# Performance work log

Hardware: AMD Instinct MI355X
Metric: run time of the kernel (lower is better)

## Reference

```python
import jax, jax.numpy as jnp
import numpy as np

K_TOP = 8
TEMP = 1.0
GUMBEL_EPS = 1e-20
GEN_EPS = 1e-7
NEG_INF = -1e9


def _genconv(xn, src, dst, e, We, be, W1, b1, W2, b2):
    """GENConv: edge-proj, m=relu(x_src+e)+eps, per-dst softmax aggregation (t=1),
    residual add, then 2-layer MLP."""
    N = xn.shape[0]
    ep = e @ We + be                         # [E, C]
    m = jax.nn.relu(xn[src] + ep) + GEN_EPS  # [E, C]
    mx = jax.ops.segment_max(m, dst, num_segments=N)
    mx = jnp.where(jnp.isfinite(mx), mx, 0.0)
    w = jnp.exp(m - mx[dst])
    den = jax.ops.segment_sum(w, dst, num_segments=N)
    agg = jax.ops.segment_sum(w * m, dst, num_segments=N) / jnp.where(den > 0, den, 1.0)
    out = agg + xn
    return jax.nn.relu(out @ W1 + b1) @ W2 + b2


def setup_inputs() -> dict:
    key = jax.random.key(0)
    ks = jax.random.split(key, 16)
    N, E, D, ED = 1024, 16384, 128, 16
    H1, H2, OUT = 64, 64, 40
    s = 0.02
    return {
        "x": jax.random.normal(ks[0], (N, D), jnp.float32),
        "edge_attr": jax.random.normal(ks[1], (E, ED), jnp.float32),
        "gumbel_u": jax.random.uniform(ks[2], (N, N), jnp.float32),
        "mlp_w": jax.random.normal(ks[3], (ED + 2 * D, 1), jnp.float32) * s,
        "mlp_b": jnp.zeros((1,), jnp.float32),
        "c1_we": jax.random.normal(ks[4], (ED, D), jnp.float32) * s,
        "c1_be": jnp.zeros((D,), jnp.float32),
        "c1_w1": jax.random.normal(ks[5], (D, 2 * D), jnp.float32) * s,
        "c1_b1": jnp.zeros((2 * D,), jnp.float32),
        "c1_w2": jax.random.normal(ks[6], (2 * D, H1), jnp.float32) * s,
        "c1_b2": jnp.zeros((H1,), jnp.float32),
        "c2_we": jax.random.normal(ks[7], (ED, H1), jnp.float32) * s,
        "c2_be": jnp.zeros((H1,), jnp.float32),
        "c2_w1": jax.random.normal(ks[8], (H1, 2 * H1), jnp.float32) * s,
        "c2_b1": jnp.zeros((2 * H1,), jnp.float32),
        "c2_w2": jax.random.normal(ks[9], (2 * H1, H2), jnp.float32) * s,
        "c2_b2": jnp.zeros((H2,), jnp.float32),
        "fc_w": jax.random.normal(ks[10], (H2, OUT), jnp.float32) * s,
        "fc_b": jnp.zeros((OUT,), jnp.float32),
        "num_nodes": N,
        "edge_index": jax.random.randint(ks[11], (2, E), 0, N),
        "node_mask": jnp.ones((N,), jnp.int32),
    }


def reference(x, edge_attr, gumbel_u, mlp_w, mlp_b,
              c1_we, c1_be, c1_w1, c1_b1, c1_w2, c1_b2,
              c2_we, c2_be, c2_w1, c2_b1, c2_w2, c2_b2,
              fc_w, fc_b, num_nodes, edge_index, node_mask):
    N, D = x.shape
    src, dst = edge_index[0], edge_index[1]

    # dense adjacency (duplicate edges sum, only used as a zero/nonzero mask)
    adj = jnp.zeros((N, N), x.dtype).at[src, dst].add(1.0)

    # Edge-score MLP on concat([x_u, x_v*mask, edge_attr_dense]) decomposed
    # linearly (same math as scoring the dense [N,N,2D+ED] feature tensor).
    w_node, w_nb, w_e = mlp_w[:D], mlp_w[D:2 * D], mlp_w[2 * D:]
    s_edge = jnp.zeros((N, N), x.dtype).at[src, dst].set((edge_attr @ w_e)[:, 0])
    score = (x @ w_node) + (x @ w_nb).T * (adj > 0) + s_edge + mlp_b[0]
    score = jnp.where(adj == 0, NEG_INF, score)

    z = jax.nn.softmax(score, axis=-1)
    g = -jnp.log(-jnp.log(gumbel_u + GUMBEL_EPS) + GUMBEL_EPS)
    z = jax.nn.softmax((z + g) / TEMP, axis=-1)

    # top-k edge sampling; softmax output is strictly positive so valid_mask
    # (z>0) is always all-True and shapes stay static at N*k edges.
    _, topi = jax.lax.top_k(z, K_TOP)                       # [N, k]
    new_src = jnp.repeat(jnp.arange(N), K_TOP)
    new_dst = topi.reshape(-1)

    # match each new edge against old edge list (argmax of boolean equality,
    # unmatched edges fall back to index 0 exactly as torch argmax does)
    eq = (edge_index[0][None, :] == new_src[:, None]) & \
         (edge_index[1][None, :] == new_dst[:, None])       # [N*k, E]
    new_attr = edge_attr[jnp.argmax(eq, axis=-1)]

    h = _genconv(x, new_src, new_dst, new_attr, c1_we, c1_be, c1_w1, c1_b1, c1_w2, c1_b2)
    h = jax.nn.relu(h)
    h = _genconv(h, new_src, new_dst, new_attr, c2_we, c2_be, c2_w1, c2_b1, c2_w2, c2_b2)
    h = jax.nn.relu(h)
    out = h @ fc_w + fc_b
    # node_mask is all ones, so x[node_mask != 0] == identity; masked write
    # keeps static shapes under jit.
    return jnp.where((node_mask != 0)[:, None], out, 0.0)
```

## Files before the change

kernel.cpp:

```cpp
#include <hip/hip_runtime.h>
#include <cfloat>

#define NN   1024
#define NE   16384
#define D0   128
#define EDIM 16
#define NH1  64
#define NOUT 40
#define KTOP 8
#define NEGINF (-1000000000.0f)

#define OFF_A    0u
#define OFF_B    4096u
#define OFF_DST  8192u
#define OFF_EM   40960u
#define OFF_H    73728u

__device__ __forceinline__ void amx(float& v, int& j, float ov, int oj) {
    if (ov > v || (ov == v && oj < j)) { v = ov; j = oj; }
}

__global__ __launch_bounds__(256) void ab_kernel(
    const float* __restrict__ x, const float* __restrict__ mlp_w,
    float* __restrict__ a, float* __restrict__ b)
{
    int t = threadIdx.x, lane = t & 63, wid = t >> 6;
    int row = blockIdx.x * 4 + wid;
    const float* xr = x + row * D0;
    float x0 = xr[lane], x1 = xr[64 + lane];
    float sa = x0 * mlp_w[lane]       + x1 * mlp_w[64 + lane];
    float sb = x0 * mlp_w[128 + lane] + x1 * mlp_w[192 + lane];
    for (int s = 32; s; s >>= 1) { sa += __shfl_down(sa, s); sb += __shfl_down(sb, s); }
    if (lane == 0) { a[row] = sa; b[row] = sb; }
}

__global__ __launch_bounds__(256) void row_topk_kernel(
    const float* __restrict__ ea, const float* __restrict__ mlp_w,
    const float* __restrict__ mlp_b, const float* __restrict__ a,
    const float* __restrict__ b, const float* __restrict__ u,
    const int* __restrict__ ei, int* __restrict__ dsti, int* __restrict__ em)
{
    __shared__ float sv[NN];
    __shared__ int   idmx[NN];
    __shared__ int   idmn[NN];
    __shared__ float wred[4];
    __shared__ int   wredj[4];
    const int i = blockIdx.x, t = threadIdx.x;
    const int lane = t & 63, wid = t >> 6;

    for (int j = t; j < NN; j += 256) { idmx[j] = -1; idmn[j] = 0x7FFFFFFF; }
    __syncthreads();
    for (int e = t; e < NE; e += 256) {
        if (ei[e] == i) {
            int dj = ei[NE + e];
            atomicMax(&idmx[dj], e);
            atomicMin(&idmn[dj], e);
        }
    }
    __syncthreads();

    float we[EDIM];
    #pragma unroll
    for (int k = 0; k < EDIM; k++) we[k] = mlp_w[2 * D0 + k];
    const float bias = mlp_b[0];
    const float ai = a[i];

    float lmax = NEGINF;
    for (int j = t; j < NN; j += 256) {
        int id = idmx[j];
        float s;
        if (id >= 0) {
            float se = 0.f;
            #pragma unroll
            for (int k = 0; k < EDIM; k++) se += ea[id * EDIM + k] * we[k];
            s = ((ai + b[j]) + se) + bias;
        } else {
            s = NEGINF;
        }
        sv[j] = s;
        lmax = fmaxf(lmax, s);
    }
    for (int s = 32; s; s >>= 1) lmax = fmaxf(lmax, __shfl_down(lmax, s));
    if (lane == 0) wred[wid] = lmax;
    __syncthreads();
    float rowmax = fmaxf(fmaxf(wred[0], wred[1]), fmaxf(wred[2], wred[3]));
    bool noedge = (rowmax == NEGINF);
    __syncthreads();

    float lsum = 0.f;
    for (int j = t; j < NN; j += 256) {
        float evv;
        if (noedge) evv = 1.0f;
        else { float s = sv[j]; evv = (s == NEGINF) ? 0.0f : expf(s - rowmax); }
        sv[j] = evv;
        lsum += evv;
    }
    for (int s = 32; s; s >>= 1) lsum += __shfl_down(lsum, s);
    if (lane == 0) wred[wid] = lsum;
    __syncthreads();
    float rsum = wred[0] + wred[1] + wred[2] + wred[3];
    __syncthreads();

    for (int j = t; j < NN; j += 256) {
        float z = sv[j] / rsum;
        float uu = u[i * NN + j];
        float g = -logf(-logf(uu + 1e-20f) + 1e-20f);
        sv[j] = z + g;
    }
    __syncthreads();

    for (int sel = 0; sel < KTOP; sel++) {
        float bv = -FLT_MAX; int bj = NN;
        for (int j = t; j < NN; j += 256) amx(bv, bj, sv[j], j);
        for (int s = 32; s; s >>= 1) {
            float ov = __shfl_down(bv, s); int oj = __shfl_down(bj, s);
            amx(bv, bj, ov, oj);
        }
        if (lane == 0) { wred[wid] = bv; wredj[wid] = bj; }
        __syncthreads();
        if (t == 0) {
            float v = wred[0]; int j = wredj[0];
            amx(v, j, wred[1], wredj[1]);
            amx(v, j, wred[2], wredj[2]);
            amx(v, j, wred[3], wredj[3]);
            dsti[i * KTOP + sel] = j;
            int mn = idmn[j];
            em[i * KTOP + sel] = (mn == 0x7FFFFFFF) ? 0 : mn;
            sv[j] = -FLT_MAX;
        }
        __syncthreads();
    }
}

__global__ __launch_bounds__(128) void genconv1_kernel(
    const float* __restrict__ x, const float* __restrict__ ea,
    const float* __restrict__ we_g, const float* __restrict__ be,
    const float* __restrict__ w1, const float* __restrict__ b1,
    const float* __restrict__ w2, const float* __restrict__ b2,
    const int* __restrict__ dsti, const int* __restrict__ em,
    float* __restrict__ h)
{
    __shared__ int   slots[256];
    __shared__ float eatt[256 * EDIM];
    __shared__ float arow[D0];
    __shared__ float t1[2 * D0];
    __shared__ int   lcnt;
    const int r = blockIdx.x, t = threadIdx.x;
    if (t == 0) lcnt = 0;
    __syncthreads();
    for (int n = t; n < NN * KTOP; n += 128)
        if (dsti[n] == r) { int p = atomicAdd(&lcnt, 1); if (p < 256) slots[p] = n; }
    __syncthreads();
    int cnt = min(lcnt, 256);
    if (t == 0) {
        for (int p = 1; p < cnt; p++) {
            int v = slots[p]; int q = p - 1;
            while (q >= 0 && slots[q] > v) { slots[q + 1] = slots[q]; q--; }
            slots[q + 1] = v;
        }
    }
    __syncthreads();
    for (int q = t; q < cnt * EDIM; q += 128)
        eatt[q] = ea[em[slots[q >> 4]] * EDIM + (q & 15)];
    __syncthreads();

    const int d = t;
    float wed[EDIM];
    #pragma unroll
    for (int k = 0; k < EDIM; k++) wed[k] = we_g[k * D0 + d];
    const float bed = be[d];

    float mxv = -FLT_MAX;
    for (int idx = 0; idx < cnt; idx++) {
        int n = slots[idx]; int src = n >> 3;
        float ep = bed;
        #pragma unroll
        for (int k = 0; k < EDIM; k++) ep += eatt[idx * EDIM + k] * wed[k];
        float m = fmaxf(x[src * D0 + d] + ep, 0.f) + 1e-7f;
        mxv = fmaxf(mxv, m);
    }
    float den = 0.f, num = 0.f;
    for (int idx = 0; idx < cnt; idx++) {
        int n = slots[idx]; int src = n >> 3;
        float ep = bed;
        #pragma unroll
        for (int k = 0; k < EDIM; k++) ep += eatt[idx * EDIM + k] * wed[k];
        float m = fmaxf(x[src * D0 + d] + ep, 0.f) + 1e-7f;
        float w = expf(m - mxv);
        den += w; num += w * m;
    }
    float agg = cnt ? num / (den > 0.f ? den : 1.f) : 0.f;
    arow[d] = agg + x[r * D0 + d];
    __syncthreads();

    float acc0 = b1[d], acc1 = b1[d + D0];
    for (int k = 0; k < D0; k++) {
        float av = arow[k];
        acc0 += av * w1[k * 2 * D0 + d];
        acc1 += av * w1[k * 2 * D0 + d + D0];
    }
    t1[d] = fmaxf(acc0, 0.f);
    t1[d + D0] = fmaxf(acc1, 0.f);
    __syncthreads();
    if (t < NH1) {
        float acc = b2[t];
        for (int k = 0; k < 2 * D0; k++) acc += t1[k] * w2[k * NH1 + t];
        h[r * NH1 + t] = fmaxf(acc, 0.f);
    }
}

__global__ __launch_bounds__(128) void genconv2_kernel(
    const float* __restrict__ h, const float* __restrict__ ea,
    const float* __restrict__ we_g, const float* __restrict__ be,
    const float* __restrict__ w1, const float* __restrict__ b1,
    const float* __restrict__ w2, const float* __restrict__ b2,
    const float* __restrict__ fcw, const float* __restrict__ fcb,
    const int* __restrict__ dsti, const int* __restrict__ em,
    const int* __restrict__ mask, float* __restrict__ out)
{
    __shared__ int   slots[256];
    __shared__ float eatt[256 * EDIM];
    __shared__ float arow[NH1];
    __shared__ float t2[2 * NH1];
    __shared__ float h2[NH1];
    __shared__ int   lcnt;
    const int r = blockIdx.x, t = threadIdx.x;
    if (t == 0) lcnt = 0;
    __syncthreads();
    for (int n = t; n < NN * KTOP; n += 128)
        if (dsti[n] == r) { int p = atomicAdd(&lcnt, 1); if (p < 256) slots[p] = n; }
    __syncthreads();
    int cnt = min(lcnt, 256);
    if (t == 0) {
        for (int p = 1; p < cnt; p++) {
            int v = slots[p]; int q = p - 1;
            while (q >= 0 && slots[q] > v) { slots[q + 1] = slots[q]; q--; }
            slots[q + 1] = v;
        }
    }
    __syncthreads();
    for (int q = t; q < cnt * EDIM; q += 128)
        eatt[q] = ea[em[slots[q >> 4]] * EDIM + (q & 15)];
    __syncthreads();

    if (t < NH1) {
        const int d = t;
        float wed[EDIM];
        #pragma unroll
        for (int k = 0; k < EDIM; k++) wed[k] = we_g[k * NH1 + d];
        const float bed = be[d];
        float mxv = -FLT_MAX;
        for (int idx = 0; idx < cnt; idx++) {
            int n = slots[idx]; int src = n >> 3;
            float ep = bed;
            #pragma unroll
            for (int k = 0; k < EDIM; k++) ep += eatt[idx * EDIM + k] * wed[k];
            float m = fmaxf(h[src * NH1 + d] + ep, 0.f) + 1e-7f;
            mxv = fmaxf(mxv, m);
        }
        float den = 0.f, num = 0.f;
        for (int idx = 0; idx < cnt; idx++) {
            int n = slots[idx]; int src = n >> 3;
            float ep = bed;
            #pragma unroll
            for (int k = 0; k < EDIM; k++) ep += eatt[idx * EDIM + k] * wed[k];
            float m = fmaxf(h[src * NH1 + d] + ep, 0.f) + 1e-7f;
            float w = expf(m - mxv);
            den += w; num += w * m;
        }
        float agg = cnt ? num / (den > 0.f ? den : 1.f) : 0.f;
        arow[d] = agg + h[r * NH1 + d];
    }
    __syncthreads();

    {
        float acc = b1[t];
        for (int k = 0; k < NH1; k++) acc += arow[k] * w1[k * 2 * NH1 + t];
        t2[t] = fmaxf(acc, 0.f);
    }
    __syncthreads();
    if (t < NH1) {
        float acc = b2[t];
        for (int k = 0; k < 2 * NH1; k++) acc += t2[k] * w2[k * NH1 + t];
        h2[t] = fmaxf(acc, 0.f);
    }
    __syncthreads();
    if (t < NOUT) {
        float acc = fcb[t];
        for (int k = 0; k < NH1; k++) acc += h2[k] * fcw[k * NOUT + t];
        out[r * NOUT + t] = (mask[r] != 0) ? acc : 0.f;
    }
}

extern "C" void kernel_launch(void* const* d_in, const int* in_sizes, int n_in,
                              void* d_out, int out_size, void* d_ws, size_t ws_size,
                              hipStream_t stream) {
    const float* x      = (const float*)d_in[0];
    const float* ea     = (const float*)d_in[1];
    const float* u      = (const float*)d_in[2];
    const float* mlp_w  = (const float*)d_in[3];
    const float* mlp_b  = (const float*)d_in[4];
    const float* c1_we  = (const float*)d_in[5];
    const float* c1_be  = (const float*)d_in[6];
    const float* c1_w1  = (const float*)d_in[7];
    const float* c1_b1  = (const float*)d_in[8];
    const float* c1_w2  = (const float*)d_in[9];
    const float* c1_b2  = (const float*)d_in[10];
    const float* c2_we  = (const float*)d_in[11];
    const float* c2_be  = (const float*)d_in[12];
    const float* c2_w1  = (const float*)d_in[13];
    const float* c2_b1  = (const float*)d_in[14];
    const float* c2_w2  = (const float*)d_in[15];
    const float* c2_b2  = (const float*)d_in[16];
    const float* fc_w   = (const float*)d_in[17];
    const float* fc_b   = (const float*)d_in[18];
    const int*   ei     = (const int*)d_in[20];
    const int*   mask   = (const int*)d_in[21];

    char* ws = (char*)d_ws;
    float* a    = (float*)(ws + OFF_A);
    float* b    = (float*)(ws + OFF_B);
    int*   dsti = (int*)(ws + OFF_DST);
    int*   em   = (int*)(ws + OFF_EM);
    float* h    = (float*)(ws + OFF_H);
    float* out  = (float*)d_out;

    ab_kernel<<<NN / 4, 256, 0, stream>>>(x, mlp_w, a, b);
    row_topk_kernel<<<NN, 256, 0, stream>>>(ea, mlp_w, mlp_b, a, b, u, ei, dsti, em);
    genconv1_kernel<<<NN, 128, 0, stream>>>(x, ea, c1_we, c1_be, c1_w1, c1_b1, c1_w2, c1_b2,
                                            dsti, em, h);
    genconv2_kernel<<<NN, 128, 0, stream>>>(h, ea, c2_we, c2_be, c2_w1, c2_b1, c2_w2, c2_b2,
                                            fc_w, fc_b, dsti, em, mask, out);
}
```

Before: 192.0 us.

## Build dense edge-id matrices and CSR incoming lists instead of per-block edge scans

Replaces each row_topk block's scan of all 16384 edges with a global dense N×N edge-id max/min table built once by atomics, and precomputes per-edge attribute scores. Adds a single-block CSR builder, so the genconv kernels read their incoming-edge lists instead of each scanning all N*k destinations. The genconv kernels now pack 2 or 4 nodes per block. This adds an 8 MB memset and a large, sparsely read table, and caps in-degree at 64, which could truncate high-degree nodes.

```diff
diff --git a/kernel.cpp b/kernel.cpp
--- a/kernel.cpp
+++ b/kernel.cpp
@@ -9,74 +9,73 @@
 #define NOUT 40
 #define KTOP 8
 #define NEGINF (-1000000000.0f)
-
-#define OFF_A    0u
-#define OFF_B    4096u
-#define OFF_DST  8192u
-#define OFF_EM   40960u
-#define OFF_H    73728u
+#define MAXDEG 64
+
+#define OFF_IDMAX 0u
+#define OFF_IDMIN 4194304u
+#define OFF_SE    8388608u
+#define OFF_A     8454144u
+#define OFF_B     8458240u
+#define OFF_DST   8462336u
+#define OFF_EM    8495104u
+#define OFF_RS    8527872u
+#define OFF_SLOT  8536064u
+#define OFF_H     8568832u
 
 __device__ __forceinline__ void amx(float& v, int& j, float ov, int oj) {
     if (ov > v || (ov == v && oj < j)) { v = ov; j = oj; }
 }
 
-__global__ __launch_bounds__(256) void ab_kernel(
-    const float* __restrict__ x, const float* __restrict__ mlp_w,
-    float* __restrict__ a, float* __restrict__ b)
-{
-    int t = threadIdx.x, lane = t & 63, wid = t >> 6;
-    int row = blockIdx.x * 4 + wid;
-    const float* xr = x + row * D0;
-    float x0 = xr[lane], x1 = xr[64 + lane];
-    float sa = x0 * mlp_w[lane]       + x1 * mlp_w[64 + lane];
-    float sb = x0 * mlp_w[128 + lane] + x1 * mlp_w[192 + lane];
-    for (int s = 32; s; s >>= 1) { sa += __shfl_down(sa, s); sb += __shfl_down(sb, s); }
-    if (lane == 0) { a[row] = sa; b[row] = sb; }
+__global__ __launch_bounds__(256) void prep_kernel(
+    const float* __restrict__ x, const float* __restrict__ ea,
+    const float* __restrict__ mlp_w, const int* __restrict__ ei,
+    int* __restrict__ idmax, unsigned* __restrict__ idmin,
+    float* __restrict__ se, float* __restrict__ a, float* __restrict__ b)
+{
+    int bid = blockIdx.x, t = threadIdx.x;
+    if (bid < 64) {
+        int e = bid * 256 + t;
+        int s = ei[e], d = ei[NE + e];
+        atomicMax(idmax + s * NN + d, e);
+        atomicMin(idmin + s * NN + d, (unsigned)e);
+        float acc = 0.f;
+        #pragma unroll
+        for (int k = 0; k < EDIM; k++) acc += ea[e * EDIM + k] * mlp_w[2 * D0 + k];
+        se[e] = acc;
+    } else {
+        int lane = t & 63, wid = t >> 6;
+        int row = (bid - 64) * 4 + wid;
+        const float* xr = x + row * D0;
+        float x0 = xr[lane], x1 = xr[64 + lane];
+        float sa = x0 * mlp_w[lane]       + x1 * mlp_w[64 + lane];
+        float sb = x0 * mlp_w[128 + lane] + x1 * mlp_w[192 + lane];
+        for (int s2 = 32; s2; s2 >>= 1) { sa += __shfl_down(sa, s2); sb += __shfl_down(sb, s2); }
+        if (lane == 0) { a[row] = sa; b[row] = sb; }
+    }
 }
 
 __global__ __launch_bounds__(256) void row_topk_kernel(
-    const float* __restrict__ ea, const float* __restrict__ mlp_w,
-    const float* __restrict__ mlp_b, const float* __restrict__ a,
-    const float* __restrict__ b, const float* __restrict__ u,
-    const int* __restrict__ ei, int* __restrict__ dsti, int* __restrict__ em)
+    const int* __restrict__ idmax, const unsigned* __restrict__ idmin,
+    const float* __restrict__ se, const float* __restrict__ mlp_b,
+    const float* __restrict__ a, const float* __restrict__ b,
+    const float* __restrict__ u, int* __restrict__ dsti, int* __restrict__ em)
 {
     __shared__ float sv[NN];
-    __shared__ int   idmx[NN];
-    __shared__ int   idmn[NN];
+    __shared__ unsigned idl[NN];
     __shared__ float wred[4];
     __shared__ int   wredj[4];
     const int i = blockIdx.x, t = threadIdx.x;
     const int lane = t & 63, wid = t >> 6;
-
-    for (int j = t; j < NN; j += 256) { idmx[j] = -1; idmn[j] = 0x7FFFFFFF; }
-    __syncthreads();
-    for (int e = t; e < NE; e += 256) {
-        if (ei[e] == i) {
-            int dj = ei[NE + e];
-            atomicMax(&idmx[dj], e);
-            atomicMin(&idmn[dj], e);
-        }
-    }
-    __syncthreads();
-
-    float we[EDIM];
-    #pragma unroll
-    for (int k = 0; k < EDIM; k++) we[k] = mlp_w[2 * D0 + k];
+    const int rowoff = i * NN;
     const float bias = mlp_b[0];
     const float ai = a[i];
 
     float lmax = NEGINF;
-    for (int j = t; j < NN; j += 256) {
-        int id = idmx[j];
-        float s;
-        if (id >= 0) {
-            float se = 0.f;
-            #pragma unroll
-            for (int k = 0; k < EDIM; k++) se += ea[id * EDIM + k] * we[k];
-            s = ((ai + b[j]) + se) + bias;
-        } else {
-            s = NEGINF;
-        }
+    #pragma unroll
+    for (int q = 0; q < 4; q++) {
+        int j = t + q * 256;
+        int id = idmax[rowoff + j];
+        float s = (id >= 0) ? (((ai + b[j]) + se[id]) + bias) : NEGINF;
         sv[j] = s;
         lmax = fmaxf(lmax, s);
     }
@@ -88,12 +87,15 @@
     __syncthreads();
 
     float lsum = 0.f;
-    for (int j = t; j < NN; j += 256) {
+    #pragma unroll
+    for (int q = 0; q < 4; q++) {
+        int j = t + q * 256;
         float evv;
         if (noedge) evv = 1.0f;
         else { float s = sv[j]; evv = (s == NEGINF) ? 0.0f : expf(s - rowmax); }
         sv[j] = evv;
         lsum += evv;
+        idl[j] = idmin[rowoff + j];
     }
     for (int s = 32; s; s >>= 1) lsum += __shfl_down(lsum, s);
     if (lane == 0) wred[wid] = lsum;
@@ -101,9 +103,11 @@
     float rsum = wred[0] + wred[1] + wred[2] + wred[3];
     __syncthreads();
 
-    for (int j = t; j < NN; j += 256) {
+    #pragma unroll
+    for (int q = 0; q < 4; q++) {
+        int j = t + q * 256;
         float z = sv[j] / rsum;
-        float uu = u[i * NN + j];
+        float uu = u[rowoff + j];
         float g = -logf(-logf(uu + 1e-20f) + 1e-20f);
         sv[j] = z + g;
     }
@@ -111,7 +115,8 @@
 
     for (int sel = 0; sel < KTOP; sel++) {
         float bv = -FLT_MAX; int bj = NN;
-        for (int j = t; j < NN; j += 256) amx(bv, bj, sv[j], j);
+        #pragma unroll
+        for (int q = 0; q < 4; q++) { int j = t + q * 256; amx(bv, bj, sv[j], j); }
         for (int s = 32; s; s >>= 1) {
             float ov = __shfl_down(bv, s); int oj = __shfl_down(bj, s);
             amx(bv, bj, ov, oj);
@@ -124,47 +129,82 @@
             amx(v, j, wred[2], wredj[2]);
             amx(v, j, wred[3], wredj[3]);
             dsti[i * KTOP + sel] = j;
-            int mn = idmn[j];
-            em[i * KTOP + sel] = (mn == 0x7FFFFFFF) ? 0 : mn;
+            unsigned mn = idl[j];
+            em[i * KTOP + sel] = (mn == 0xFFFFFFFFu) ? 0 : (int)mn;
             sv[j] = -FLT_MAX;
         }
         __syncthreads();
     }
 }
 
-__global__ __launch_bounds__(128) void genconv1_kernel(
+__global__ __launch_bounds__(1024) void csr_kernel(
+    const int* __restrict__ dsti, int* __restrict__ rs, int* __restrict__ slot)
+{
+    __shared__ int cnts[NN];
+    __shared__ int sc[NN];
+    __shared__ int ptr[NN];
+    const int t = threadIdx.x;
+    cnts[t] = 0;
+    __syncthreads();
+    int dloc[8];
+    #pragma unroll
+    for (int q = 0; q < 8; q++) {
+        dloc[q] = dsti[q * NN + t];
+        atomicAdd(&cnts[dloc[q]], 1);
+    }
+    __syncthreads();
+    int v = cnts[t];
+    sc[t] = v;
+    __syncthreads();
+    for (int off = 1; off < NN; off <<= 1) {
+        int add = (t >= off) ? sc[t - off] : 0;
+        __syncthreads();
+        sc[t] += add;
+        __syncthreads();
+    }
+    int excl = sc[t] - v;
+    rs[t] = excl;
+    if (t == NN - 1) rs[NN] = NE / 2;
+    ptr[t] = excl;
+    __syncthreads();
+    #pragma unroll
+    for (int q = 0; q < 8; q++) {
+        int n = q * NN + t;
+        int p = atomicAdd(&ptr[dloc[q]], 1);
+        slot[p] = n;
+    }
+}
+
+__global__ __launch_bounds__(256) void genconv1_kernel(
     const float* __restrict__ x, const float* __restrict__ ea,
     const float* __restrict__ we_g, const float* __restrict__ be,
     const float* __restrict__ w1, const float* __restrict__ b1,
     const float* __restrict__ w2, const float* __restrict__ b2,
-    const int* __restrict__ dsti, const int* __restrict__ em,
-    float* __restrict__ h)
-{
-    __shared__ int   slots[256];
-    __shared__ float eatt[256 * EDIM];
-    __shared__ float arow[D0];
-    __shared__ float t1[2 * D0];
-    __shared__ int   lcnt;
-    const int r = blockIdx.x, t = threadIdx.x;
-    if (t == 0) lcnt = 0;
-    __syncthreads();
-    for (int n = t; n < NN * KTOP; n += 128)
-        if (dsti[n] == r) { int p = atomicAdd(&lcnt, 1); if (p < 256) slots[p] = n; }
-    __syncthreads();
-    int cnt = min(lcnt, 256);
-    if (t == 0) {
+    const int* __restrict__ rs, const int* __restrict__ slot,
+    const int* __restrict__ em, float* __restrict__ h)
+{
+    __shared__ int   slots[2][MAXDEG];
+    __shared__ float eatt[2][MAXDEG * EDIM];
+    __shared__ float arow[2][D0];
+    __shared__ float t1s[2][2 * D0];
+    const int t = threadIdx.x, sub = t >> 7, d = t & 127;
+    const int r = blockIdx.x * 2 + sub;
+    const int beg = rs[r];
+    const int cnt = min(rs[r + 1] - beg, MAXDEG);
+    if (d < cnt) slots[sub][d] = slot[beg + d];
+    __syncthreads();
+    if (d == 0) {
         for (int p = 1; p < cnt; p++) {
-            int v = slots[p]; int q = p - 1;
-            while (q >= 0 && slots[q] > v) { slots[q + 1] = slots[q]; q--; }
-            slots[q + 1] = v;
-        }
-    }
-    __syncthreads();
-    for (int q = t; q < cnt * EDIM; q += 128)
-        eatt[q] = ea[em[slots[q >> 4]] * EDIM + (q & 15)];
-    __syncthreads();
-
-    const int d = t;
+            int v = slots[sub][p]; int q = p - 1;
+            while (q >= 0 && slots[sub][q] > v) { slots[sub][q + 1] = slots[sub][q]; q--; }
+            slots[sub][q + 1] = v;
+        }
+    }
+    __syncthreads();
+    for (int q = d; q < cnt * EDIM; q += 128)
+        eatt[sub][q] = ea[em[slots[sub][q >> 4]] * EDIM + (q & 15)];
+    __syncthreads();
+
     float wed[EDIM];
     #pragma unroll
     for (int k = 0; k < EDIM; k++) wed[k] = we_g[k * D0 + d];
@@ -172,123 +212,125 @@
 
     float mxv = -FLT_MAX;
     for (int idx = 0; idx < cnt; idx++) {
-        int n = slots[idx]; int src = n >> 3;
+        int src = slots[sub][idx] >> 3;
         float ep = bed;
         #pragma unroll
-        for (int k = 0; k < EDIM; k++) ep += eatt[idx * EDIM + k] * wed[k];
+        for (int k = 0; k < EDIM; k++) ep += eatt[sub][idx * EDIM + k] * wed[k];
         float m = fmaxf(x[src * D0 + d] + ep, 0.f) + 1e-7f;
         mxv = fmaxf(mxv, m);
     }
     float den = 0.f, num = 0.f;
     for (int idx = 0; idx < cnt; idx++) {
-        int n = slots[idx]; int src = n >> 3;
+        int src = slots[sub][idx] >> 3;
         float ep = bed;
         #pragma unroll
-        for (int k = 0; k < EDIM; k++) ep += eatt[idx * EDIM + k] * wed[k];
+        for (int k = 0; k < EDIM; k++) ep += eatt[sub][idx * EDIM + k] * wed[k];
         float m = fmaxf(x[src * D0 + d] + ep, 0.f) + 1e-7f;
         float w = expf(m - mxv);
         den += w; num += w * m;
     }
     float agg = cnt ? num / (den > 0.f ? den : 1.f) : 0.f;
-    arow[d] = agg + x[r * D0 + d];
+    arow[sub][d] = agg + x[r * D0 + d];
     __syncthreads();
 
     float acc0 = b1[d], acc1 = b1[d + D0];
     for (int k = 0; k < D0; k++) {
-        float av = arow[k];
+        float av = arow[sub][k];
         acc0 += av * w1[k * 2 * D0 + d];
         acc1 += av * w1[k * 2 * D0 + d + D0];
     }
-    t1[d] = fmaxf(acc0, 0.f);
-    t1[d + D0] = fmaxf(acc1, 0.f);
-    __syncthreads();
-    if (t < NH1) {
-        float acc = b2[t];
-        for (int k = 0; k < 2 * D0; k++) acc += t1[k] * w2[k * NH1 + t];
-        h[r * NH1 + t] = fmaxf(acc, 0.f);
-    }
-}
-
-__global__ __launch_bounds__(128) void genconv2_kernel(
+    t1s[sub][d] = fmaxf(acc0, 0.f);
+    t1s[sub][d + D0] = fmaxf(acc1, 0.f);
+    __syncthreads();
+    if (d < NH1) {
+        float acc = b2[d];
+        for (int k = 0; k < 2 * D0; k++) acc += t1s[sub][k] * w2[k * NH1 + d];
+        h[r * NH1 + d] = fmaxf(acc, 0.f);
+    }
+}
+
+__global__ __launch_bounds__(256) void genconv2_kernel(
     const float* __restrict__ h, const float* __restrict__ ea,
     const float* __restrict__ we_g, const float* __restrict__ be,
     const float* __restrict__ w1, const float* __restrict__ b1,
     const float* __restrict__ w2, const float* __restrict__ b2,
     const float* __restrict__ fcw, const float* __restrict__ fcb,
-    const int* __restrict__ dsti, const int* __restrict__ em,
-    const int* __restrict__ mask, float* __restrict__ out)
-{
-    __shared__ int   slots[256];
-    __shared__ float eatt[256 * EDIM];
-    __shared__ float arow[NH1];
-    __shared__ float t2[2 * NH1];
-    __shared__ float h2[NH1];
-    __shared__ int   lcnt;
-    const int r = blockIdx.x, t = threadIdx.x;
-    if (t == 0) lcnt = 0;
-    __syncthreads();
-    for (int n = t; n < NN * KTOP; n += 128)
-        if (dsti[n] == r) { int p = atomicAdd(&lcnt, 1); if (p < 256) slots[p] = n; }
-    __syncthreads();
-    int cnt = min(lcnt, 256);
-    if (t == 0) {
+    const int* __restrict__ rs, const int* __restrict__ slot,
+    const int* __restrict__ em, const int* __restrict__ mask,
+    float* __restrict__ out)
+{
+    __shared__ int   slots[4][MAXDEG];
+    __shared__ float eatt[4][MAXDEG * EDIM];
+    __shared__ float arow[4][NH1];
+    __shared__ float t2s[4][2 * NH1];
+    __shared__ float h2s[4][NH1];
+    const int t = threadIdx.x, sub = t >> 6, d = t & 63;
+    const int r = blockIdx.x * 4 + sub;
+    const int beg = rs[r];
+    const int cnt = min(rs[r + 1] - beg, MAXDEG);
+    if (d < cnt) slots[sub][d] = slot[beg + d];
+    __syncthreads();
+    if (d == 0) {
         for (int p = 1; p < cnt; p++) {
-            int v = slots[p]; int q = p - 1;
-            while (q >= 0 && slots[q] > v) { slots[q + 1] = slots[q]; q--; }
-            slots[q + 1] = v;
-        }
-    }
-    __syncthreads();
-    for (int q = t; q < cnt * EDIM; q += 128)
-        eatt[q] = ea[em[slots[q >> 4]] * EDIM + (q & 15)];
-    __syncthreads();
-
-    if (t < NH1) {
-        const int d = t;
-        float wed[EDIM];
-        #pragma unroll
-        for (int k = 0; k < EDIM; k++) wed[k] = we_g[k * NH1 + d];
-        const float bed = be[d];
-        float mxv = -FLT_MAX;
-        for (int idx = 0; idx < cnt; idx++) {
-            int n = slots[idx]; int src = n >> 3;
-            float ep = bed;
-            #pragma unroll
-            for (int k = 0; k < EDIM; k++) ep += eatt[idx * EDIM + k] * wed[k];
-            float m = fmaxf(h[src * NH1 + d] + ep, 0.f) + 1e-7f;
-            mxv = fmaxf(mxv, m);
-        }
-        float den = 0.f, num = 0.f;
-        for (int idx = 0; idx < cnt; idx++) {
-            int n = slots[idx]; int src = n >> 3;
-            float ep = bed;
-            #pragma unroll
-            for (int k = 0; k < EDIM; k++) ep += eatt[idx * EDIM + k] * wed[k];
-            float m = fmaxf(h[src * NH1 + d] + ep, 0.f) + 1e-7f;
-            float w = expf(m - mxv);
-            den += w; num += w * m;
-        }
-        float agg = cnt ? num / (den > 0.f ? den : 1.f) : 0.f;
-        arow[d] = agg + h[r * NH1 + d];
-    }
+            int v = slots[sub][p]; int q = p - 1;
+            while (q >= 0 && slots[sub][q] > v) { slots[sub][q + 1] = slots[sub][q]; q--; }
+            slots[sub][q + 1] = v;
+        }
+    }
+    __syncthreads();
+    for (int q = d; q < cnt * EDIM; q += 64)
+        eatt[sub][q] = ea[em[slots[sub][q >> 4]] * EDIM + (q & 15)];
+    __syncthreads();
+
+    float wed[EDIM];
+    #pragma unroll
+    for (int k = 0; k < EDIM; k++) wed[k] = we_g[k * NH1 + d];
+    const float bed = be[d];
+
+    float mxv = -FLT_MAX;
+    for (int idx = 0; idx < cnt; idx++) {
+        int src = slots[sub][idx] >> 3;
+        float ep = bed;
+        #pragma unroll
+        for (int k = 0; k < EDIM; k++) ep += eatt[sub][idx * EDIM + k] * wed[k];
+        float m = fmaxf(h[src * NH1 + d] + ep, 0.f) + 1e-7f;
+        mxv = fmaxf(mxv, m);
+    }
+    float den = 0.f, num = 0.f;
+    for (int idx = 0; idx < cnt; idx++) {
+        int src = slots[sub][idx] >> 3;
+        float ep = bed;
+        #pragma unroll
+        for (int k = 0; k < EDIM; k++) ep += eatt[sub][idx * EDIM + k] * wed[k];
+        float m = fmaxf(h[src * NH1 + d] + ep, 0.f) + 1e-7f;
+        float w = expf(m - mxv);
+        den += w; num += w * m;
+    }
+    float agg = cnt ? num / (den > 0.f ? den : 1.f) : 0.f;
+    arow[sub][d] = agg + h[r * NH1 + d];
     __syncthreads();
 
     {
-        float acc = b1[t];
-        for (int k = 0; k < NH1; k++) acc += arow[k] * w1[k * 2 * NH1 + t];
-        t2[t] = fmaxf(acc, 0.f);
-    }
-    __syncthreads();
-    if (t < NH1) {
-        float acc = b2[t];
-        for (int k = 0; k < 2 * NH1; k++) acc += t2[k] * w2[k * NH1 + t];
-        h2[t] = fmaxf(acc, 0.f);
-    }
-    __syncthreads();
-    if (t < NOUT) {
-        float acc = fcb[t];
-        for (int k = 0; k < NH1; k++) acc += h2[k] * fcw[k * NOUT + t];
-        out[r * NOUT + t] = (mask[r] != 0) ? acc : 0.f;
+        float acc_a = b1[d], acc_b = b1[d + NH1];
+        for (int k = 0; k < NH1; k++) {
+            float av = arow[sub][k];
+            acc_a += av * w1[k * 2 * NH1 + d];
+            acc_b += av * w1[k * 2 * NH1 + d + NH1];
+        }
+        t2s[sub][d] = fmaxf(acc_a, 0.f);
+        t2s[sub][d + NH1] = fmaxf(acc_b, 0.f);
+    }
+    __syncthreads();
+    {
+        float acc = b2[d];
+        for (int k = 0; k < 2 * NH1; k++) acc += t2s[sub][k] * w2[k * NH1 + d];
+        h2s[sub][d] = fmaxf(acc, 0.f);
+    }
+    __syncthreads();
+    if (d < NOUT) {
+        float acc = fcb[d];
+        for (int k = 0; k < NH1; k++) acc += h2s[sub][k] * fcw[k * NOUT + d];
+        out[r * NOUT + d] = (mask[r] != 0) ? acc : 0.f;
     }
 }
 
@@ -318,17 +360,24 @@
     const int*   mask   = (const int*)d_in[21];
 
     char* ws = (char*)d_ws;
+    int*      idmax = (int*)(ws + OFF_IDMAX);
+    unsigned* idmin = (unsigned*)(ws + OFF_IDMIN);
+    float* se   = (float*)(ws + OFF_SE);
     float* a    = (float*)(ws + OFF_A);
     float* b    = (float*)(ws + OFF_B);
     int*   dsti = (int*)(ws + OFF_DST);
     int*   em   = (int*)(ws + OFF_EM);
+    int*   rs   = (int*)(ws + OFF_RS);
+    int*   slot = (int*)(ws + OFF_SLOT);
     float* h    = (float*)(ws + OFF_H);
     float* out  = (float*)d_out;
 
-    ab_kernel<<<NN / 4, 256, 0, stream>>>(x, mlp_w, a, b);
-    row_topk_kernel<<<NN, 256, 0, stream>>>(ea, mlp_w, mlp_b, a, b, u, ei, dsti, em);
-    genconv1_kernel<<<NN, 128, 0, stream>>>(x, ea, c1_we, c1_be, c1_w1, c1_b1, c1_w2, c1_b2,
-                                            dsti, em, h);
-    genconv2_kernel<<<NN, 128, 0, stream>>>(h, ea, c2_we, c2_be, c2_w1, c2_b1, c2_w2, c2_b2,
-                                            fc_w, fc_b, dsti, em, mask, out);
-}
+    hipMemsetAsync(ws + OFF_IDMAX, 0xFF, 8388608u, stream);
+    prep_kernel<<<320, 256, 0, stream>>>(x, ea, mlp_w, ei, idmax, idmin, se, a, b);
+    row_topk_kernel<<<NN, 256, 0, stream>>>(idmax, idmin, se, mlp_b, a, b, u, dsti, em);
+    csr_kernel<<<1, 1024, 0, stream>>>(dsti, rs, slot);
+    genconv1_kernel<<<NN / 2, 256, 0, stream>>>(x, ea, c1_we, c1_be, c1_w1, c1_b1, c1_w2, c1_b2,
+                                                rs, slot, em, h);
+    genconv2_kernel<<<NN / 4, 256, 0, stream>>>(h, ea, c2_we, c2_be, c2_w1, c2_b1, c2_w2, c2_b2,
+                                                fc_w, fc_b, rs, slot, em, mask, out);
+}
```

Result: faster. 165.3 us (-13.9%).
